# Kernel optimization log

Hardware: AMD Instinct MI355X
Metric: run time of the kernel (lower is better)

The kernel has to match this reference:

```python
import jax, jax.numpy as jnp
import numpy as np

WIN = 7
N_HEADS = 12


def _swin_rel_pos_index(win_h, win_w):
    # standard Swin relative position index, flattened to (win_h*win_w)**2
    coords = np.stack(np.meshgrid(np.arange(win_h), np.arange(win_w), indexing='ij'))  # 2, Wh, Ww
    coords_flat = coords.reshape(2, -1)
    rel = coords_flat[:, :, None] - coords_flat[:, None, :]  # 2, N, N
    rel = rel.transpose(1, 2, 0).astype(np.int64)
    rel[:, :, 0] += win_h - 1
    rel[:, :, 1] += win_w - 1
    rel[:, :, 0] *= 2 * win_w - 1
    return rel.sum(-1).reshape(-1).astype(np.int32)  # (N*N,)


def setup_inputs() -> dict:
    key = jax.random.key(0)
    ks = jax.random.split(key, 8)
    B_, N, C = 4096, WIN * WIN, 384
    num_win = 64
    x = jax.random.normal(ks[0], (B_, N, C), dtype=jnp.float32)
    # 0 / -inf style additive mask (use -100 like Swin's masked_fill value)
    m = jax.random.uniform(ks[1], (num_win, N, N))
    mask = jnp.where(m < 0.5, 0.0, -100.0).astype(jnp.float32)
    qkv_w = jax.random.normal(ks[2], (3 * C, C), dtype=jnp.float32) * 0.02
    qkv_b = jax.random.normal(ks[3], (3 * C,), dtype=jnp.float32) * 0.02
    proj_w = jax.random.normal(ks[4], (C, C), dtype=jnp.float32) * 0.02
    proj_b = jax.random.normal(ks[5], (C,), dtype=jnp.float32) * 0.02
    bias_table = jax.random.normal(ks[6], ((2 * WIN - 1) ** 2, N_HEADS), dtype=jnp.float32) * 0.02
    rel_index = jnp.asarray(_swin_rel_pos_index(WIN, WIN))
    return {"x": x, "mask": mask, "qkv_w": qkv_w, "qkv_b": qkv_b,
            "proj_w": proj_w, "proj_b": proj_b, "bias_table": bias_table,
            "rel_index": rel_index}


def reference(x, mask, qkv_w, qkv_b, proj_w, proj_b, bias_table, rel_index):
    B_, N, C = x.shape
    H = N_HEADS
    hd = C // H
    scale = hd ** (-0.5)
    # qkv projection: (B_, N, 3C) -> (3, B_, H, N, hd)
    qkv = (jnp.einsum('bnc,oc->bno', x, qkv_w) + qkv_b)
    qkv = qkv.reshape(B_, N, 3, H, hd).transpose(2, 0, 3, 1, 4)
    q, k, v = qkv[0] * scale, qkv[1], qkv[2]
    attn = jnp.einsum('bhnd,bhmd->bhnm', q, k)  # (B_, H, N, N)
    # relative position bias gather: (N*N, H) -> (H, N, N)
    bias = bias_table[rel_index].reshape(N, N, H).transpose(2, 0, 1)
    attn = attn + bias[None]
    num_win = mask.shape[0]
    attn = attn.reshape(B_ // num_win, num_win, H, N, N) + mask[None, :, None]
    attn = attn.reshape(B_, H, N, N)
    attn = jax.nn.softmax(attn, axis=-1)
    out = jnp.einsum('bhnm,bhmd->bnhd', attn, v).reshape(B_, N, H * hd)
    out = jnp.einsum('bnc,oc->bno', out, proj_w) + proj_b
    return out
```

## Files before the change

kernel.cpp:

```cpp
#include <hip/hip_runtime.h>
#include <hip/hip_bf16.h>
#include <stdint.h>
#include <stddef.h>


typedef __attribute__((ext_vector_type(8))) __bf16 bf16x8;
typedef __attribute__((ext_vector_type(4))) float f32x4;
typedef __attribute__((ext_vector_type(4))) unsigned short u16x4;
typedef __attribute__((ext_vector_type(8))) unsigned short u16x8;

typedef const unsigned int __attribute__((address_space(1)))* gptr_t;
typedef unsigned int __attribute__((address_space(3)))* lptr_t;

#define SCALE 0.17677669529663687f

__device__ __forceinline__ unsigned short f2bf(float f) {
  union { float f; unsigned int u; } c; c.f = f;
  unsigned int r = c.u + 0x7fffu + ((c.u >> 16) & 1u);
  return (unsigned short)(r >> 16);
}

__device__ __forceinline__ void gl_lds16(const void* g, void* s) {
  __builtin_amdgcn_global_load_lds((gptr_t)g, (lptr_t)s, 16, 0, 0);
}

__global__ __launch_bounds__(256) void convert_kernel(
    const float* __restrict__ x, unsigned short* __restrict__ xb, long nx4,
    const float* __restrict__ w1, unsigned short* __restrict__ w1b, long n14,
    const float* __restrict__ w2, unsigned short* __restrict__ w2b, long n24) {
  long stride = (long)gridDim.x * blockDim.x;
  long t0 = (long)blockIdx.x * blockDim.x + threadIdx.x;
  for (long i = t0; i < nx4; i += stride) {
    f32x4 v = ((const f32x4*)x)[i];
    u16x4 o;
#pragma unroll
    for (int j = 0; j < 4; ++j) o[j] = f2bf(v[j]);
    ((u16x4*)xb)[i] = o;
  }
  for (long i = t0; i < n14; i += stride) {
    f32x4 v = ((const f32x4*)w1)[i];
    u16x4 o;
#pragma unroll
    for (int j = 0; j < 4; ++j) o[j] = f2bf(v[j]);
    ((u16x4*)w1b)[i] = o;
  }
  for (long i = t0; i < n24; i += stride) {
    f32x4 v = ((const f32x4*)w2)[i];
    u16x4 o;
#pragma unroll
    for (int j = 0; j < 4; ++j) o[j] = f2bf(v[j]);
    ((u16x4*)w2b)[i] = o;
  }
}

__global__ __launch_bounds__(256) void cmb_kernel(
    const float* __restrict__ mask, const float* __restrict__ bias_table,
    const int* __restrict__ rel_index, float* __restrict__ cmb) {
  int idx = blockIdx.x * 256 + threadIdx.x;
  int j = idx & 63, i = (idx >> 6) & 63;
  int hw = idx >> 12;
  int h = hw % 12, w = hw / 12;
  float v = -1e30f;
  if (i < 49 && j < 49)
    v = bias_table[rel_index[i * 49 + j] * 12 + h] + mask[(w * 49 + i) * 49 + j];
  cmb[idx] = v;
}

template <int NBN, int KDIM, bool OUT_BF16>
__global__ __launch_bounds__(256) void gemm_nt(
    const unsigned short* __restrict__ A, const unsigned short* __restrict__ Bw,
    const float* __restrict__ bias, unsigned short* __restrict__ Cb,
    float* __restrict__ Cf, int Nn) {
  __shared__ __align__(16) unsigned short Sm[24576];
  const int tid = threadIdx.x;
  const int w = tid >> 6, l = tid & 63, q = l >> 4, ln = l & 15;
  const int cpx = gridDim.x >> 3;
  const int swz = (blockIdx.x & 7) * cpx + (blockIdx.x >> 3);
  const int bm = swz / NBN, bn = swz % NBN;
  const unsigned short* Ab = A + (size_t)bm * 128 * KDIM;
  const unsigned short* Bb = Bw + (size_t)bn * 128 * KDIM;
  const int wm = w >> 1, wn = w & 1;
  const int lrow = l >> 2;
  const int lch = (l & 3) ^ ((l >> 3) & 3);

  float bv[4];
#pragma unroll
  for (int j = 0; j < 4; ++j) bv[j] = bias[bn * 128 + wn * 64 + j * 16 + ln];

  auto stage = [&](int buf, int k0) {
    unsigned short* as = Sm + buf * 4096;
    unsigned short* bs = Sm + 12288 + buf * 4096;
#pragma unroll
    for (int i = 0; i < 2; ++i) {
      int rowbase = (w * 2 + i) * 16;
      gl_lds16(Ab + (size_t)(rowbase + lrow) * KDIM + k0 + lch * 8,
               &as[rowbase * 32]);
      gl_lds16(Bb + (size_t)(rowbase + lrow) * KDIM + k0 + lch * 8,
               &bs[rowbase * 32]);
    }
  };

  f32x4 acc[4][4] = {};
  const int ch = q ^ ((ln >> 1) & 3);
  constexpr int NIT = KDIM / 32;
  stage(0, 0);
  stage(1, 32);
#pragma unroll
  for (int t = 0; t < NIT; ++t) {
    if (t + 2 < NIT) {
      stage((t + 2) % 3, (t + 2) * 32);
      asm volatile("s_waitcnt vmcnt(8)" ::: "memory");
    } else if (t + 1 < NIT) {
      asm volatile("s_waitcnt vmcnt(4)" ::: "memory");
    } else {
      asm volatile("s_waitcnt vmcnt(0)" ::: "memory");
    }
    __builtin_amdgcn_s_barrier();
    const unsigned short* as = Sm + (t % 3) * 4096;
    const unsigned short* bs = Sm + 12288 + (t % 3) * 4096;
    bf16x8 af[4], bf[4];
#pragma unroll
    for (int tt = 0; tt < 4; ++tt) {
      af[tt] = *(const bf16x8*)&as[(wm * 64 + tt * 16 + ln) * 32 + ch * 8];
      bf[tt] = *(const bf16x8*)&bs[(wn * 64 + tt * 16 + ln) * 32 + ch * 8];
    }
#pragma unroll
    for (int i = 0; i < 4; ++i)
#pragma unroll
      for (int j = 0; j < 4; ++j)
        acc[i][j] = __builtin_amdgcn_mfma_f32_16x16x32_bf16(af[i], bf[j],
                                                            acc[i][j], 0, 0, 0);
    asm volatile("s_waitcnt lgkmcnt(0)" ::: "memory");
    __builtin_amdgcn_s_barrier();
  }

  if constexpr (OUT_BF16) {
    const int rr = tid >> 4, c8 = (tid & 15) * 8;
    const size_t crow = (size_t)bm * 128;
#pragma unroll
    for (int half = 0; half < 2; ++half) {
      if (wm == half) {
#pragma unroll
        for (int j = 0; j < 4; ++j) {
          int col = wn * 64 + j * 16 + ln;
#pragma unroll
          for (int i = 0; i < 4; ++i) {
            int r0 = i * 16 + q * 4;
#pragma unroll
            for (int r = 0; r < 4; ++r)
              Sm[(r0 + r) * 132 + col] = f2bf(acc[i][j][r] + bv[j]);
          }
        }
      }
      __syncthreads();
#pragma unroll
      for (int p = 0; p < 4; ++p) {
        int row = p * 16 + rr;
        u16x4 v0 = *(const u16x4*)&Sm[row * 132 + c8];
        u16x4 v1 = *(const u16x4*)&Sm[row * 132 + c8 + 4];
        u16x8 v;
#pragma unroll
        for (int k = 0; k < 4; ++k) { v[k] = v0[k]; v[4 + k] = v1[k]; }
        *(u16x8*)&Cb[(crow + half * 64 + row) * Nn + bn * 128 + c8] = v;
      }
      if (half == 0) __syncthreads();
    }
  } else {
#pragma unroll
    for (int j = 0; j < 4; ++j) {
      int col = bn * 128 + wn * 64 + j * 16 + ln;
#pragma unroll
      for (int i = 0; i < 4; ++i) {
        int row0 = bm * 128 + wm * 64 + i * 16 + q * 4;
#pragma unroll
        for (int r = 0; r < 4; ++r)
          Cf[(size_t)(row0 + r) * Nn + col] = acc[i][j][r] + bv[j];
      }
    }
  }
}

__global__ __launch_bounds__(256) void attn_kernel(
    const unsigned short* __restrict__ qkv, const float* __restrict__ cmb,
    unsigned short* __restrict__ aout) {
  __shared__ __align__(16) unsigned short Ps[4][64 * 80];
  const int tid = threadIdx.x;
  const int w = tid >> 6, l = tid & 63, q = l >> 4, ln = l & 15;
  const int pair = blockIdx.x * 4 + w;
  const int b = pair / 12, h = pair % 12;
  const int win = b & 63;
  const unsigned short* base = qkv + (size_t)b * 49 * 1152 + h * 32;
  bf16x8 qf[4], kf[4];
#pragma unroll
  for (int t = 0; t < 4; ++t) {
    int r = t * 16 + ln;
    int rr = (r < 49) ? r : 0;
    qf[t] = *(const bf16x8*)(base + (size_t)rr * 1152 + q * 8);
    kf[t] = *(const bf16x8*)(base + 384 + (size_t)rr * 1152 + q * 8);
  }
  f32x4 s[4][4] = {};
#pragma unroll
  for (int i = 0; i < 4; ++i)
#pragma unroll
    for (int j = 0; j < 4; ++j)
      s[i][j] = __builtin_amdgcn_mfma_f32_16x16x32_bf16(qf[i], kf[j], s[i][j],
                                                        0, 0, 0);
  const float* cb = cmb + ((size_t)win * 12 + h) * 4096;
#pragma unroll
  for (int mt = 0; mt < 4; ++mt) {
#pragma unroll
    for (int r = 0; r < 4; ++r) {
      int row = mt * 16 + q * 4 + r;
      float v[4];
#pragma unroll
      for (int nt = 0; nt < 4; ++nt)
        v[nt] = s[mt][nt][r] * SCALE + cb[row * 64 + nt * 16 + ln];
      float m = fmaxf(fmaxf(v[0], v[1]), fmaxf(v[2], v[3]));
#pragma unroll
      for (int off = 1; off < 16; off <<= 1)
        m = fmaxf(m, __shfl_xor(m, off, 64));
      float p[4], sum = 0.f;
#pragma unroll
      for (int nt = 0; nt < 4; ++nt) { p[nt] = __expf(v[nt] - m); sum += p[nt]; }
#pragma unroll
      for (int off = 1; off < 16; off <<= 1)
        sum += __shfl_xor(sum, off, 64);
      float inv = 1.0f / sum;
#pragma unroll
      for (int nt = 0; nt < 4; ++nt)
        Ps[w][row * 80 + nt * 16 + ln] = f2bf(p[nt] * inv);
    }
  }
  __syncthreads();
  const __bf16* vbase = (const __bf16*)(base + 768);
  bf16x8 vf[2][2];
#pragma unroll
  for (int nt = 0; nt < 2; ++nt)
#pragma unroll
    for (int kt = 0; kt < 2; ++kt) {
      bf16x8 tmp;
#pragma unroll
      for (int jj = 0; jj < 8; ++jj) {
        int j = kt * 32 + q * 8 + jj;
        int jc = (j < 49) ? j : 0;
        tmp[jj] = vbase[(size_t)jc * 1152 + nt * 16 + ln];
      }
      vf[nt][kt] = tmp;
    }
  f32x4 o[4][2] = {};
#pragma unroll
  for (int mt = 0; mt < 4; ++mt)
#pragma unroll
    for (int kt = 0; kt < 2; ++kt) {
      bf16x8 pf = *(const bf16x8*)&Ps[w][(mt * 16 + ln) * 80 + kt * 32 + q * 8];
#pragma unroll
      for (int nt = 0; nt < 2; ++nt)
        o[mt][nt] = __builtin_amdgcn_mfma_f32_16x16x32_bf16(pf, vf[nt][kt],
                                                            o[mt][nt], 0, 0, 0);
    }
#pragma unroll
  for (int mt = 0; mt < 4; ++mt)
#pragma unroll
    for (int r = 0; r < 4; ++r) {
      int n = mt * 16 + q * 4 + r;
      if (n < 49) {
#pragma unroll
        for (int nt = 0; nt < 2; ++nt)
          aout[((size_t)b * 49 + n) * 384 + h * 32 + nt * 16 + ln] =
              f2bf(o[mt][nt][r]);
      }
    }
}

extern "C" void kernel_launch(void* const* d_in, const int* in_sizes, int n_in,
                              void* d_out, int out_size, void* d_ws,
                              size_t ws_size, hipStream_t stream) {
  (void)in_sizes; (void)n_in; (void)out_size; (void)ws_size;
  const float* x          = (const float*)d_in[0];
  const float* mask       = (const float*)d_in[1];
  const float* qkv_w      = (const float*)d_in[2];
  const float* qkv_b      = (const float*)d_in[3];
  const float* proj_w     = (const float*)d_in[4];
  const float* proj_b     = (const float*)d_in[5];
  const float* bias_table = (const float*)d_in[6];
  const int*   rel_index  = (const int*)d_in[7];

  char* ws = (char*)d_ws;
  unsigned short* qkv  = (unsigned short*)ws;
  unsigned short* xb   = (unsigned short*)(ws + 462422016ull);
  unsigned short* aout = xb;
  unsigned short* wq   = (unsigned short*)(ws + 616562688ull);
  unsigned short* wp   = (unsigned short*)(ws + 617447424ull);
  float*          cmb  = (float*)(ws + 617742336ull);

  convert_kernel<<<2048, 256, 0, stream>>>(x, xb, 19267584L,
                                           qkv_w, wq, 110592L,
                                           proj_w, wp, 36864L);
  cmb_kernel<<<12288, 256, 0, stream>>>(mask, bias_table, rel_index, cmb);
  gemm_nt<9, 384, true><<<14112, 256, 0, stream>>>(xb, wq, qkv_b, qkv, nullptr,
                                                   1152);
  attn_kernel<<<12288, 256, 0, stream>>>(qkv, cmb, aout);
  gemm_nt<3, 384, false><<<4704, 256, 0, stream>>>(aout, wp, proj_b, nullptr,
                                                   (float*)d_out, 384);
}
```

Measured before the change: 1.226 ms.

## Enlarge GEMM tiles to 256x128 with 8 waves and split-phase double buffering

Doubles the GEMM block tile along M to 256 rows using 512 threads (8 waves), widens the K step to 64 with an XOR-swizzled 64-column LDS layout, and replaces the triple-buffered 32-wide pipeline with a double buffer. Each K step is split into two MFMA phases, with next-tile loads issued between them, raised wave priority during MFMA, and A loads spread across wave parity. The aim is more reuse of the B tile per load, fewer barriers per unit of K, and better overlap of global-to-LDS copies with compute. In exchange the block uses twice the LDS and more registers, which lowers occupancy, and the hand-counted vmcnt waits must match the new load counts exactly.

```diff
diff --git a/kernel.cpp b/kernel.cpp
--- a/kernel.cpp
+++ b/kernel.cpp
@@ -67,79 +67,129 @@
 }
 
 template <int NBN, int KDIM, bool OUT_BF16>
-__global__ __launch_bounds__(256) void gemm_nt(
+__global__ __launch_bounds__(512) void gemm_nt(
     const unsigned short* __restrict__ A, const unsigned short* __restrict__ Bw,
     const float* __restrict__ bias, unsigned short* __restrict__ Cb,
     float* __restrict__ Cf, int Nn) {
-  __shared__ __align__(16) unsigned short Sm[24576];
+  __shared__ __align__(16) unsigned short Sm[49152];
   const int tid = threadIdx.x;
   const int w = tid >> 6, l = tid & 63, q = l >> 4, ln = l & 15;
   const int cpx = gridDim.x >> 3;
   const int swz = (blockIdx.x & 7) * cpx + (blockIdx.x >> 3);
   const int bm = swz / NBN, bn = swz % NBN;
-  const unsigned short* Ab = A + (size_t)bm * 128 * KDIM;
+  const unsigned short* Ab = A + (size_t)bm * 256 * KDIM;
   const unsigned short* Bb = Bw + (size_t)bn * 128 * KDIM;
   const int wm = w >> 1, wn = w & 1;
-  const int lrow = l >> 2;
-  const int lch = (l & 3) ^ ((l >> 3) & 3);
+  const int srow = l >> 3;
+  const int sch = (l & 7) ^ srow;
 
   float bv[4];
 #pragma unroll
   for (int j = 0; j < 4; ++j) bv[j] = bias[bn * 128 + wn * 64 + j * 16 + ln];
 
-  auto stage = [&](int buf, int k0) {
-    unsigned short* as = Sm + buf * 4096;
-    unsigned short* bs = Sm + 12288 + buf * 4096;
-#pragma unroll
-    for (int i = 0; i < 2; ++i) {
-      int rowbase = (w * 2 + i) * 16;
-      gl_lds16(Ab + (size_t)(rowbase + lrow) * KDIM + k0 + lch * 8,
-               &as[rowbase * 32]);
-      gl_lds16(Bb + (size_t)(rowbase + lrow) * KDIM + k0 + lch * 8,
-               &bs[rowbase * 32]);
-    }
+  auto stageA = [&](int buf, int k0, int i) {
+    int r0 = w * 32 + i * 8;
+    gl_lds16(Ab + (size_t)(r0 + srow) * KDIM + k0 + sch * 8,
+             Sm + buf * 16384 + r0 * 64);
   };
+  auto stageB = [&](int buf, int k0, int i) {
+    int r0 = w * 16 + i * 8;
+    gl_lds16(Bb + (size_t)(r0 + srow) * KDIM + k0 + sch * 8,
+             Sm + 32768 + buf * 8192 + r0 * 64);
+  };
+  auto ldA = [&](int buf, int fr, int ks) -> bf16x8 {
+    int r = wm * 64 + fr * 16 + ln;
+    int c = (ks * 4 + q) ^ (r & 7);
+    return *(const bf16x8*)(Sm + buf * 16384 + r * 64 + c * 8);
+  };
+  auto ldB = [&](int buf, int fc, int ks) -> bf16x8 {
+    int r = wn * 64 + fc * 16 + ln;
+    int c = (ks * 4 + q) ^ (r & 7);
+    return *(const bf16x8*)(Sm + 32768 + buf * 8192 + r * 64 + c * 8);
+  };
 
   f32x4 acc[4][4] = {};
-  const int ch = q ^ ((ln >> 1) & 3);
-  constexpr int NIT = KDIM / 32;
-  stage(0, 0);
-  stage(1, 32);
+  constexpr int NIT = KDIM / 64;
+
+#pragma unroll
+  for (int i = 0; i < 4; ++i) stageA(0, 0, i);
+#pragma unroll
+  for (int i = 0; i < 2; ++i) stageB(0, 0, i);
+  if (!(w & 1)) {
+#pragma unroll
+    for (int i = 0; i < 4; ++i) stageA(1, 64, i);
+  }
+#pragma unroll
+  for (int i = 0; i < 2; ++i) stageB(1, 64, i);
+
 #pragma unroll
   for (int t = 0; t < NIT; ++t) {
+    const int buf = t & 1, nbuf = buf ^ 1;
+    if ((w & 1) && t + 1 < NIT) {
+#pragma unroll
+      for (int i = 0; i < 4; ++i) stageA(nbuf, (t + 1) * 64, i);
+    }
+    if (t + 1 < NIT)
+      asm volatile("s_waitcnt vmcnt(6)" ::: "memory");
+    else
+      asm volatile("s_waitcnt vmcnt(0)" ::: "memory");
+    __builtin_amdgcn_s_barrier();
+    bf16x8 bfr[4][2], afr[2][2];
+#pragma unroll
+    for (int fc = 0; fc < 4; ++fc)
+#pragma unroll
+      for (int ks = 0; ks < 2; ++ks) bfr[fc][ks] = ldB(buf, fc, ks);
+#pragma unroll
+    for (int fr = 0; fr < 2; ++fr)
+#pragma unroll
+      for (int ks = 0; ks < 2; ++ks) afr[fr][ks] = ldA(buf, fr, ks);
+    asm volatile("s_waitcnt lgkmcnt(0)" ::: "memory");
+    __builtin_amdgcn_sched_barrier(0);
+    __builtin_amdgcn_s_setprio(1);
+#pragma unroll
+    for (int ks = 0; ks < 2; ++ks)
+#pragma unroll
+      for (int fr = 0; fr < 2; ++fr)
+#pragma unroll
+        for (int fc = 0; fc < 4; ++fc)
+          acc[fr][fc] = __builtin_amdgcn_mfma_f32_16x16x32_bf16(
+              afr[fr][ks], bfr[fc][ks], acc[fr][fc], 0, 0, 0);
+    __builtin_amdgcn_s_setprio(0);
+    __builtin_amdgcn_s_barrier();
+    bf16x8 af2[2][2];
+#pragma unroll
+    for (int fr = 0; fr < 2; ++fr)
+#pragma unroll
+      for (int ks = 0; ks < 2; ++ks) af2[fr][ks] = ldA(buf, 2 + fr, ks);
     if (t + 2 < NIT) {
-      stage((t + 2) % 3, (t + 2) * 32);
-      asm volatile("s_waitcnt vmcnt(8)" ::: "memory");
-    } else if (t + 1 < NIT) {
-      asm volatile("s_waitcnt vmcnt(4)" ::: "memory");
-    } else {
-      asm volatile("s_waitcnt vmcnt(0)" ::: "memory");
-    }
+      if (!(w & 1)) {
+#pragma unroll
+        for (int i = 0; i < 4; ++i) stageA(buf, (t + 2) * 64, i);
+      }
+#pragma unroll
+      for (int i = 0; i < 2; ++i) stageB(buf, (t + 2) * 64, i);
+    }
+    asm volatile("s_waitcnt lgkmcnt(0)" ::: "memory");
+    __builtin_amdgcn_sched_barrier(0);
+    __builtin_amdgcn_s_setprio(1);
+#pragma unroll
+    for (int ks = 0; ks < 2; ++ks)
+#pragma unroll
+      for (int fr = 0; fr < 2; ++fr)
+#pragma unroll
+        for (int fc = 0; fc < 4; ++fc)
+          acc[2 + fr][fc] = __builtin_amdgcn_mfma_f32_16x16x32_bf16(
+              af2[fr][ks], bfr[fc][ks], acc[2 + fr][fc], 0, 0, 0);
+    __builtin_amdgcn_s_setprio(0);
     __builtin_amdgcn_s_barrier();
-    const unsigned short* as = Sm + (t % 3) * 4096;
-    const unsigned short* bs = Sm + 12288 + (t % 3) * 4096;
-    bf16x8 af[4], bf[4];
-#pragma unroll
-    for (int tt = 0; tt < 4; ++tt) {
-      af[tt] = *(const bf16x8*)&as[(wm * 64 + tt * 16 + ln) * 32 + ch * 8];
-      bf[tt] = *(const bf16x8*)&bs[(wn * 64 + tt * 16 + ln) * 32 + ch * 8];
-    }
-#pragma unroll
-    for (int i = 0; i < 4; ++i)
-#pragma unroll
-      for (int j = 0; j < 4; ++j)
-        acc[i][j] = __builtin_amdgcn_mfma_f32_16x16x32_bf16(af[i], bf[j],
-                                                            acc[i][j], 0, 0, 0);
-    asm volatile("s_waitcnt lgkmcnt(0)" ::: "memory");
-    __builtin_amdgcn_s_barrier();
   }
 
   if constexpr (OUT_BF16) {
-    const int rr = tid >> 4, c8 = (tid & 15) * 8;
-    const size_t crow = (size_t)bm * 128;
-#pragma unroll
-    for (int half = 0; half < 2; ++half) {
-      if (wm == half) {
+    const int rr = tid >> 3, c0 = (tid & 7) * 8;
+    const size_t crow = (size_t)bm * 256;
+#pragma unroll
+    for (int h = 0; h < 4; ++h) {
+      if (wm == h) {
 #pragma unroll
         for (int j = 0; j < 4; ++j) {
           int col = wn * 64 + j * 16 + ln;
@@ -154,16 +204,16 @@
       }
       __syncthreads();
 #pragma unroll
-      for (int p = 0; p < 4; ++p) {
-        int row = p * 16 + rr;
-        u16x4 v0 = *(const u16x4*)&Sm[row * 132 + c8];
-        u16x4 v1 = *(const u16x4*)&Sm[row * 132 + c8 + 4];
+      for (int part = 0; part < 2; ++part) {
+        int c = c0 + part * 64;
+        u16x4 v0 = *(const u16x4*)&Sm[rr * 132 + c];
+        u16x4 v1 = *(const u16x4*)&Sm[rr * 132 + c + 4];
         u16x8 v;
 #pragma unroll
         for (int k = 0; k < 4; ++k) { v[k] = v0[k]; v[4 + k] = v1[k]; }
-        *(u16x8*)&Cb[(crow + half * 64 + row) * Nn + bn * 128 + c8] = v;
-      }
-      if (half == 0) __syncthreads();
+        *(u16x8*)&Cb[(crow + h * 64 + rr) * Nn + bn * 128 + c] = v;
+      }
+      if (h < 3) __syncthreads();
     }
   } else {
 #pragma unroll
@@ -171,7 +221,7 @@
       int col = bn * 128 + wn * 64 + j * 16 + ln;
 #pragma unroll
       for (int i = 0; i < 4; ++i) {
-        int row0 = bm * 128 + wm * 64 + i * 16 + q * 4;
+        int row0 = bm * 256 + wm * 64 + i * 16 + q * 4;
 #pragma unroll
         for (int r = 0; r < 4; ++r)
           Cf[(size_t)(row0 + r) * Nn + col] = acc[i][j][r] + bv[j];
@@ -297,9 +347,9 @@
                                            qkv_w, wq, 110592L,
                                            proj_w, wp, 36864L);
   cmb_kernel<<<12288, 256, 0, stream>>>(mask, bias_table, rel_index, cmb);
-  gemm_nt<9, 384, true><<<14112, 256, 0, stream>>>(xb, wq, qkv_b, qkv, nullptr,
-                                                   1152);
+  gemm_nt<9, 384, true><<<7056, 512, 0, stream>>>(xb, wq, qkv_b, qkv, nullptr,
+                                                  1152);
   attn_kernel<<<12288, 256, 0, stream>>>(qkv, cmb, aout);
-  gemm_nt<3, 384, false><<<4704, 256, 0, stream>>>(aout, wp, proj_b, nullptr,
+  gemm_nt<3, 384, false><<<2352, 512, 0, stream>>>(aout, wp, proj_b, nullptr,
                                                    (float*)d_out, 384);
 }
```

Measured after the change: 1.226 ms. Within noise of the previous version (+0.0%).
